# Performance work log

Measured on AMD Instinct MI355X. Metric: run time of the kernel, lower is better.

The kernel has to match this reference:

```python
import jax, jax.numpy as jnp
import numpy as np

EPS = 1e-5

def _conv1d(x, w, b):
    # x: [B, T, Cin]; w: [Cout, Cin, K] (torch layout); padding=1, stride=1
    y = jax.lax.conv_general_dilated(
        x, jnp.transpose(w, (2, 1, 0)), window_strides=(1,), padding=[(1, 1)],
        dimension_numbers=('NWC', 'WIO', 'NWC'))
    return y + b

def _layernorm(x, g, b):
    mu = jnp.mean(x, axis=-1, keepdims=True)
    var = jnp.mean(jnp.square(x - mu), axis=-1, keepdims=True)
    return (x - mu) * jax.lax.rsqrt(var + EPS) * g + b

def _predictor(x, conv1_w, conv1_b, ln1_g, ln1_b, conv2_w, conv2_b, ln2_g, ln2_b, lin_w, lin_b):
    h = _layernorm(jax.nn.relu(_conv1d(x, conv1_w, conv1_b)), ln1_g, ln1_b)
    h = _layernorm(jax.nn.relu(_conv1d(h, conv2_w, conv2_b)), ln2_g, ln2_b)
    # linear to 1 channel, relu, squeeze -> [B, T]
    return jax.nn.relu(jnp.einsum('btf,f->bt', h, lin_w[:, 0]) + lin_b[0])

def _length_regulate(x, durations, mel_max_length):
    # Equivalent to the one-hot alignment matmul: output frame p of batch b
    # copies token k where cumsum(dur)[k-1] <= p < cumsum(dur)[k]; zeros beyond total.
    B, T, D = x.shape
    cum = jnp.cumsum(durations, axis=-1)                       # [B, T]
    frames = jnp.arange(mel_max_length, dtype=cum.dtype)       # [M]
    idx = jax.vmap(lambda c: jnp.searchsorted(c, frames, side='right'))(cum)  # [B, M]
    idx = jnp.clip(idx, 0, T - 1)
    out = jnp.take_along_axis(x, idx[..., None], axis=1)       # [B, M, D]
    mask = (frames[None, :] < cum[:, -1:])                     # [B, M]
    return out * mask[..., None].astype(x.dtype)

def setup_inputs() -> dict:
    key = jax.random.key(0)
    ks = jax.random.split(key, 8)
    B, T, D, F = 32, 512, 256, 256
    M = 3584  # mel_max_length >= max possible sum of durations (7 * 512)
    x = jax.random.normal(ks[0], (B, T, D), dtype=jnp.float32)
    target = jax.random.randint(ks[1], (B, T), 0, 8, dtype=jnp.int32)
    s = 0.02
    return {
        'x': x,
        'conv1_w': jax.random.normal(ks[2], (F, D, 3), jnp.float32) * s,
        'conv1_b': jnp.zeros((F,), jnp.float32),
        'ln1_g': jnp.ones((F,), jnp.float32),
        'ln1_b': jnp.zeros((F,), jnp.float32),
        'conv2_w': jax.random.normal(ks[3], (F, F, 3), jnp.float32) * s,
        'conv2_b': jnp.zeros((F,), jnp.float32),
        'ln2_g': jnp.ones((F,), jnp.float32),
        'ln2_b': jnp.zeros((F,), jnp.float32),
        'lin_w': jax.random.normal(ks[4], (F, 1), jnp.float32) * s,
        'lin_b': jnp.zeros((1,), jnp.float32),
        'target': target,
        'mel_max_length': M,
    }

def reference(x, conv1_w, conv1_b, ln1_g, ln1_b, conv2_w, conv2_b, ln2_g, ln2_b, lin_w, lin_b, target, mel_max_length):
    dur_pred = _predictor(x, conv1_w, conv1_b, ln1_g, ln1_b, conv2_w, conv2_b, ln2_g, ln2_b, lin_w, lin_b)
    output = _length_regulate(x, target, mel_max_length)
    return output, dur_pred
```

## Files before the change

kernel.cpp:

```cpp
#include <hip/hip_runtime.h>
#include <hip/hip_bf16.h>

typedef float f32x4 __attribute__((ext_vector_type(4)));
typedef __bf16 bf16x8 __attribute__((ext_vector_type(8)));

static __device__ __forceinline__ unsigned short f2bf(float f) {
    unsigned int u = __float_as_uint(f);
    unsigned int r = (u + 0x7fffu + ((u >> 16) & 1u)) >> 16;
    return (unsigned short)r;
}

static __device__ __forceinline__ void gll16(const void* g, void* l) {
    __builtin_amdgcn_global_load_lds(
        (const __attribute__((address_space(1))) unsigned int*)g,
        (__attribute__((address_space(3))) unsigned int*)l, 16, 0, 0);
}

__global__ __launch_bounds__(512) void prep(
    const float* __restrict__ w1, const float* __restrict__ w2,
    unsigned short* __restrict__ w1p, unsigned short* __restrict__ w2p,
    const int* __restrict__ tgt, short* __restrict__ idxT, int M)
{
    int blk = blockIdx.x;
    if (blk < 768) {
        int gi = blk * 512 + threadIdx.x;
        const float* w = (gi < 196608) ? w1 : w2;
        unsigned short* wp = (gi < 196608) ? w1p : w2p;
        int j = (gi < 196608) ? gi : gi - 196608;
        int e = j & 7;
        int ch = j >> 3;
        int kt = ch >> 10;
        int rem = ch & 1023;
        int nb = rem >> 6, l = rem & 63;
        int n = nb * 16 + (l & 15);
        int cin = (kt & 7) * 32 + (l >> 4) * 8 + e;
        int kk = kt >> 3;
        wp[j] = f2bf(w[n * 768 + cin * 3 + kk]);
    } else {
        __shared__ int s[512];
        int b = blk - 768, tid = threadIdx.x;
        int d = tgt[b * 512 + tid];
        s[tid] = d;
        __syncthreads();
        for (int off = 1; off < 512; off <<= 1) {
            int v = (tid >= off) ? s[tid - off] : 0;
            __syncthreads();
            s[tid] += v;
            __syncthreads();
        }
        int myend = s[tid];
        int mystart = myend - d;
        short* row = idxT + (size_t)b * M;
        for (int p = mystart; p < myend; ++p) row[p] = (short)tid;
        __syncthreads();
        int total = s[511];
        for (int p = total + tid; p < M; p += 512) row[p] = (short)-1;
    }
}

static __device__ __forceinline__ void gather_part(
    int gblk, int phase, const float* __restrict__ x, const short* __restrict__ idxT,
    float* __restrict__ out, int M, int wv, int lane)
{
    int b = gblk / 56;
    int r0 = (gblk % 56) * 32 + phase;
    const short* row = idxT + (size_t)b * M;
    int id[4];
    #pragma unroll
    for (int i = 0; i < 4; ++i) id[i] = row[r0 + i * 8 + wv];
    #pragma unroll
    for (int i = 0; i < 4; ++i) {
        int m = r0 + i * 8 + wv;
        float4 v = make_float4(0.f, 0.f, 0.f, 0.f);
        if (id[i] >= 0)
            v = *reinterpret_cast<const float4*>(x + ((size_t)(b * 512 + id[i])) * 256 + lane * 4);
        *reinterpret_cast<float4*>(out + ((size_t)b * M + m) * 256 + lane * 4) = v;
    }
}

__global__ __launch_bounds__(512, 4) void conv1_hetero(
    const float* __restrict__ x, const unsigned short* __restrict__ Wp,
    const float* __restrict__ bias, const float* __restrict__ g,
    const float* __restrict__ be, unsigned short* __restrict__ h1b,
    const short* __restrict__ idxT, float* __restrict__ out, int M)
{
    __shared__ __align__(16) unsigned short As[66 * 256];
    __shared__ __align__(16) unsigned short Bsm[2][8192];
    __shared__ float lnS[4][64], lnQ[4][64];

    const int tid = threadIdx.x;
    const int lane = tid & 63;
    const int wv = tid >> 6;

    if (blockIdx.x >= 256) {
        gather_part(blockIdx.x - 256, 0, x, idxT, out, M, wv, lane);
        return;
    }

    const int wmi = wv >> 2, wni = wv & 3;
    const int grp = lane >> 4, lr = lane & 15;
    const int b = blockIdx.x >> 3;
    const int t_base = (blockIdx.x & 7) * 64;

    #pragma unroll
    for (int i = 0; i < 9; ++i) {
        int cc = i * 512 + tid;
        if (cc < 66 * 64) {
            int row = cc >> 6, q = cc & 63;
            int tt = t_base - 1 + row;
            ushort4 o = make_ushort4(0, 0, 0, 0);
            if ((unsigned)tt < 512u) {
                float4 v = *reinterpret_cast<const float4*>(x + ((size_t)(b * 512 + tt)) * 256 + q * 4);
                o.x = f2bf(v.x); o.y = f2bf(v.y); o.z = f2bf(v.z); o.w = f2bf(v.w);
            }
            *reinterpret_cast<ushort4*>(&As[row * 256 + ((q * 4) ^ ((row & 7) << 3))]) = o;
        }
    }

    const char* wpB = (const char*)Wp;
    char* bs0 = (char*)&Bsm[0][0];
    #define STAGE_B(kt, buf) do {                                              \
        const char* _s = wpB + (kt) * 16384 + wv * 2048 + lane * 16;           \
        char* _d = bs0 + (buf) * 16384 + wv * 2048;                            \
        gll16(_s, _d); gll16(_s + 1024, _d + 1024);                            \
    } while (0)

    STAGE_B(0, 0);
    __syncthreads();

    f32x4 acc[2][4] = {};
    int cur = 0;
    for (int kt = 0; kt < 24; ++kt) {
        if (kt < 23) STAGE_B(kt + 1, cur ^ 1);
        const int kk = kt >> 3, cin0 = (kt & 7) * 32;
        bf16x8 af[2], bfr[4];
        #pragma unroll
        for (int mi = 0; mi < 2; ++mi) {
            int tr = wmi * 32 + mi * 16 + lr + kk;
            af[mi] = *reinterpret_cast<const bf16x8*>(&As[tr * 256 + ((cin0 + grp * 8) ^ ((tr & 7) << 3))]);
        }
        #pragma unroll
        for (int ni = 0; ni < 4; ++ni)
            bfr[ni] = *reinterpret_cast<const bf16x8*>(&Bsm[cur][(wni * 4 + ni) * 512 + lane * 8]);
        __builtin_amdgcn_s_setprio(1);
        #pragma unroll
        for (int mi = 0; mi < 2; ++mi)
            #pragma unroll
            for (int ni = 0; ni < 4; ++ni)
                acc[mi][ni] = __builtin_amdgcn_mfma_f32_16x16x32_bf16(af[mi], bfr[ni], acc[mi][ni], 0, 0, 0);
        __builtin_amdgcn_s_setprio(0);
        __syncthreads();
        cur ^= 1;
    }

    float bcol[4], gcol[4], becol[4];
    #pragma unroll
    for (int ni = 0; ni < 4; ++ni) {
        int col = wni * 64 + ni * 16 + lr;
        bcol[ni] = bias[col]; gcol[ni] = g[col]; becol[ni] = be[col];
    }
    #pragma unroll
    for (int mi = 0; mi < 2; ++mi)
        #pragma unroll
        for (int ni = 0; ni < 4; ++ni)
            #pragma unroll
            for (int r = 0; r < 4; ++r)
                acc[mi][ni][r] = fmaxf(acc[mi][ni][r] + bcol[ni], 0.f);

    #pragma unroll
    for (int mi = 0; mi < 2; ++mi)
        #pragma unroll
        for (int r = 0; r < 4; ++r) {
            float s = acc[mi][0][r] + acc[mi][1][r] + acc[mi][2][r] + acc[mi][3][r];
            float q = acc[mi][0][r] * acc[mi][0][r] + acc[mi][1][r] * acc[mi][1][r]
                    + acc[mi][2][r] * acc[mi][2][r] + acc[mi][3][r] * acc[mi][3][r];
            #pragma unroll
            for (int off = 1; off < 16; off <<= 1) {
                s += __shfl_xor(s, off);
                q += __shfl_xor(q, off);
            }
            if (lr == 0) {
                int R = wmi * 32 + mi * 16 + grp * 4 + r;
                lnS[wni][R] = s; lnQ[wni][R] = q;
            }
        }
    __syncthreads();

    unsigned short* Hs = &Bsm[0][0];
    #pragma unroll
    for (int mi = 0; mi < 2; ++mi)
        #pragma unroll
        for (int r = 0; r < 4; ++r) {
            int R = wmi * 32 + mi * 16 + grp * 4 + r;
            float mu = (lnS[0][R] + lnS[1][R] + lnS[2][R] + lnS[3][R]) * (1.f / 256.f);
            float var = (lnQ[0][R] + lnQ[1][R] + lnQ[2][R] + lnQ[3][R]) * (1.f / 256.f) - mu * mu;
            float rs = rsqrtf(var + 1e-5f);
            #pragma unroll
            for (int ni = 0; ni < 4; ++ni) {
                int col = wni * 64 + ni * 16 + lr;
                float h = (acc[mi][ni][r] - mu) * rs * gcol[ni] + becol[ni];
                Hs[R * 256 + (col ^ ((R & 7) << 3))] = f2bf(h);
            }
        }
    __syncthreads();
    #pragma unroll
    for (int i = 0; i < 4; ++i) {
        int c = i * 512 + tid;
        int row = c >> 5, seg = c & 31;
        uint4 v = *reinterpret_cast<const uint4*>(&Hs[row * 256 + seg * 8]);
        *reinterpret_cast<uint4*>(h1b + ((size_t)(b * 512 + t_base + row)) * 256 + seg * 8) = v;
    }
    #undef STAGE_B
}

__global__ __launch_bounds__(512, 4) void conv2_hetero(
    const unsigned short* __restrict__ h1b, const unsigned short* __restrict__ Wp,
    const float* __restrict__ bias, const float* __restrict__ g,
    const float* __restrict__ be, const float* __restrict__ lw,
    const float* __restrict__ lb, float* __restrict__ dur,
    const short* __restrict__ idxT, const float* __restrict__ x,
    float* __restrict__ out, int M)
{
    __shared__ __align__(16) unsigned short As[66 * 256];
    __shared__ __align__(16) unsigned short Bsm[2][8192];
    __shared__ float lnS[4][64], lnQ[4][64], lnD[4][64];

    const int tid = threadIdx.x;
    const int lane = tid & 63;
    const int wv = tid >> 6;

    if (blockIdx.x >= 256) {
        gather_part(blockIdx.x - 256, 1792, x, idxT, out, M, wv, lane);
        return;
    }

    const int wmi = wv >> 2, wni = wv & 3;
    const int grp = lane >> 4, lr = lane & 15;
    const int b = blockIdx.x >> 3;
    const int t_base = (blockIdx.x & 7) * 64;

    {
        const char* src = (const char*)h1b + ((size_t)(b * 512 + t_base)) * 512 + wv * 4096 + lane * 16;
        char* dst = (char*)&As[256] + wv * 4096;
        #pragma unroll
        for (int i = 0; i < 4; ++i) gll16(src + i * 1024, dst + i * 1024);
    }
    if (tid < 32) {
        int tt = t_base - 1;
        uint4 v = make_uint4(0u, 0u, 0u, 0u);
        if (tt >= 0)
            v = *reinterpret_cast<const uint4*>((const char*)h1b + ((size_t)(b * 512 + tt)) * 512 + tid * 16);
        *reinterpret_cast<uint4*>((char*)As + tid * 16) = v;
    } else if (tid < 64) {
        int t2 = tid - 32, tt = t_base + 64;
        uint4 v = make_uint4(0u, 0u, 0u, 0u);
        if (tt < 512)
            v = *reinterpret_cast<const uint4*>((const char*)h1b + ((size_t)(b * 512 + tt)) * 512 + t2 * 16);
        *reinterpret_cast<uint4*>((char*)&As[65 * 256] + t2 * 16) = v;
    }

    const char* wpB = (const char*)Wp;
    char* bs0 = (char*)&Bsm[0][0];
    #define STAGE_B(kt, buf) do {                                              \
        const char* _s = wpB + (kt) * 16384 + wv * 2048 + lane * 16;           \
        char* _d = bs0 + (buf) * 16384 + wv * 2048;                            \
        gll16(_s, _d); gll16(_s + 1024, _d + 1024);                            \
    } while (0)

    STAGE_B(0, 0);
    __syncthreads();

    f32x4 acc[2][4] = {};
    int cur = 0;
    for (int kt = 0; kt < 24; ++kt) {
        if (kt < 23) STAGE_B(kt + 1, cur ^ 1);
        const int kk = kt >> 3, cin0 = (kt & 7) * 32;
        bf16x8 af[2], bfr[4];
        #pragma unroll
        for (int mi = 0; mi < 2; ++mi) {
            int tr = wmi * 32 + mi * 16 + lr + kk;
            af[mi] = *reinterpret_cast<const bf16x8*>(&As[tr * 256 + ((cin0 + grp * 8) ^ (((tr + 7) & 7) << 3))]);
        }
        #pragma unroll
        for (int ni = 0; ni < 4; ++ni)
            bfr[ni] = *reinterpret_cast<const bf16x8*>(&Bsm[cur][(wni * 4 + ni) * 512 + lane * 8]);
        __builtin_amdgcn_s_setprio(1);
        #pragma unroll
        for (int mi = 0; mi < 2; ++mi)
            #pragma unroll
            for (int ni = 0; ni < 4; ++ni)
                acc[mi][ni] = __builtin_amdgcn_mfma_f32_16x16x32_bf16(af[mi], bfr[ni], acc[mi][ni], 0, 0, 0);
        __builtin_amdgcn_s_setprio(0);
        __syncthreads();
        cur ^= 1;
    }

    float bcol[4], gcol[4], becol[4], wcol[4];
    #pragma unroll
    for (int ni = 0; ni < 4; ++ni) {
        int col = wni * 64 + ni * 16 + lr;
        bcol[ni] = bias[col]; gcol[ni] = g[col]; becol[ni] = be[col]; wcol[ni] = lw[col];
    }
    #pragma unroll
    for (int mi = 0; mi < 2; ++mi)
        #pragma unroll
        for (int ni = 0; ni < 4; ++ni)
            #pragma unroll
            for (int r = 0; r < 4; ++r)
                acc[mi][ni][r] = fmaxf(acc[mi][ni][r] + bcol[ni], 0.f);

    #pragma unroll
    for (int mi = 0; mi < 2; ++mi)
        #pragma unroll
        for (int r = 0; r < 4; ++r) {
            float s = acc[mi][0][r] + acc[mi][1][r] + acc[mi][2][r] + acc[mi][3][r];
            float q = acc[mi][0][r] * acc[mi][0][r] + acc[mi][1][r] * acc[mi][1][r]
                    + acc[mi][2][r] * acc[mi][2][r] + acc[mi][3][r] * acc[mi][3][r];
            #pragma unroll
            for (int off = 1; off < 16; off <<= 1) {
                s += __shfl_xor(s, off);
                q += __shfl_xor(q, off);
            }
            if (lr == 0) {
                int R = wmi * 32 + mi * 16 + grp * 4 + r;
                lnS[wni][R] = s; lnQ[wni][R] = q;
            }
        }
    __syncthreads();
    #pragma unroll
    for (int mi = 0; mi < 2; ++mi)
        #pragma unroll
        for (int r = 0; r < 4; ++r) {
            int R = wmi * 32 + mi * 16 + grp * 4 + r;
            float mu = (lnS[0][R] + lnS[1][R] + lnS[2][R] + lnS[3][R]) * (1.f / 256.f);
            float var = (lnQ[0][R] + lnQ[1][R] + lnQ[2][R] + lnQ[3][R]) * (1.f / 256.f) - mu * mu;
            float rs = rsqrtf(var + 1e-5f);
            float d = ((acc[mi][0][r] - mu) * rs * gcol[0] + becol[0]) * wcol[0]
                    + ((acc[mi][1][r] - mu) * rs * gcol[1] + becol[1]) * wcol[1]
                    + ((acc[mi][2][r] - mu) * rs * gcol[2] + becol[2]) * wcol[2]
                    + ((acc[mi][3][r] - mu) * rs * gcol[3] + becol[3]) * wcol[3];
            #pragma unroll
            for (int off = 1; off < 16; off <<= 1) d += __shfl_xor(d, off);
            if (lr == 0) lnD[wni][R] = d;
        }
    __syncthreads();
    if (tid < 64) {
        float dd = lnD[0][tid] + lnD[1][tid] + lnD[2][tid] + lnD[3][tid] + lb[0];
        dur[(size_t)b * 512 + t_base + tid] = fmaxf(dd, 0.f);
    }
    #undef STAGE_B
}

extern "C" void kernel_launch(void* const* d_in, const int* in_sizes, int n_in,
                              void* d_out, int out_size, void* d_ws, size_t ws_size,
                              hipStream_t stream) {
    const float* x   = (const float*)d_in[0];
    const float* w1  = (const float*)d_in[1];
    const float* b1  = (const float*)d_in[2];
    const float* g1  = (const float*)d_in[3];
    const float* be1 = (const float*)d_in[4];
    const float* w2  = (const float*)d_in[5];
    const float* b2  = (const float*)d_in[6];
    const float* g2  = (const float*)d_in[7];
    const float* be2 = (const float*)d_in[8];
    const float* lw  = (const float*)d_in[9];
    const float* lb  = (const float*)d_in[10];
    const int* tgt   = (const int*)d_in[11];
    float* out = (float*)d_out;

    const int B = 32, T = 512, C = 256;
    const int rows = B * T;
    const int M = (out_size - rows) / (B * C);

    char* ws = (char*)d_ws;
    unsigned short* w1p = (unsigned short*)(ws);
    unsigned short* w2p = (unsigned short*)(ws + 393216);
    unsigned short* h1b = (unsigned short*)(ws + 786432);
    short* idxT         = (short*)(ws + 9175040);

    prep<<<800, 512, 0, stream>>>(w1, w2, w1p, w2p, tgt, idxT, M);
    conv1_hetero<<<2048, 512, 0, stream>>>(x, w1p, b1, g1, be1, h1b, idxT, out, M);
    conv2_hetero<<<2048, 512, 0, stream>>>(h1b, w2p, b2, g2, be2, lw, lb,
                                           out + (size_t)B * M * C, idxT, x, out, M);
}
```

Baseline: 58.49 us.

## Single-buffer weight tiles for higher occupancy, coalesce weight prep, nontemporal gather stores

```diff
diff --git a/kernel.cpp b/kernel.cpp
--- a/kernel.cpp
+++ b/kernel.cpp
@@ -22,23 +22,23 @@
     const int* __restrict__ tgt, short* __restrict__ idxT, int M)
 {
     int blk = blockIdx.x;
-    if (blk < 768) {
+    if (blk < 256) {
         int gi = blk * 512 + threadIdx.x;
-        const float* w = (gi < 196608) ? w1 : w2;
-        unsigned short* wp = (gi < 196608) ? w1p : w2p;
-        int j = (gi < 196608) ? gi : gi - 196608;
-        int e = j & 7;
-        int ch = j >> 3;
-        int kt = ch >> 10;
-        int rem = ch & 1023;
-        int nb = rem >> 6, l = rem & 63;
-        int n = nb * 16 + (l & 15);
-        int cin = (kt & 7) * 32 + (l >> 4) * 8 + e;
-        int kk = kt >> 3;
-        wp[j] = f2bf(w[n * 768 + cin * 3 + kk]);
+        const float* w = (gi < 65536) ? w1 : w2;
+        unsigned short* wp = (gi < 65536) ? w1p : w2p;
+        int p = gi & 65535;
+        int n = p >> 8, cin = p & 255;
+        const float* src = w + (size_t)p * 3;
+        float a[3] = {src[0], src[1], src[2]};
+        int nb = n >> 4, nl = n & 15;
+        int e = cin & 7, lhi = (cin >> 3) & 3, chi = cin >> 5;
+        int base = nb * 512 + (lhi * 16 + nl) * 8 + e;
+        #pragma unroll
+        for (int kk = 0; kk < 3; ++kk)
+            wp[(kk * 8 + chi) * 8192 + base] = f2bf(a[kk]);
     } else {
         __shared__ int s[512];
-        int b = blk - 768, tid = threadIdx.x;
+        int b = blk - 256, tid = threadIdx.x;
         int d = tgt[b * 512 + tid];
         s[tid] = d;
         __syncthreads();
@@ -71,21 +71,22 @@
     #pragma unroll
     for (int i = 0; i < 4; ++i) {
         int m = r0 + i * 8 + wv;
-        float4 v = make_float4(0.f, 0.f, 0.f, 0.f);
+        f32x4 v = {0.f, 0.f, 0.f, 0.f};
         if (id[i] >= 0)
-            v = *reinterpret_cast<const float4*>(x + ((size_t)(b * 512 + id[i])) * 256 + lane * 4);
-        *reinterpret_cast<float4*>(out + ((size_t)b * M + m) * 256 + lane * 4) = v;
-    }
-}
-
-__global__ __launch_bounds__(512, 4) void conv1_hetero(
+            v = *reinterpret_cast<const f32x4*>(x + ((size_t)(b * 512 + id[i])) * 256 + lane * 4);
+        __builtin_nontemporal_store(
+            v, reinterpret_cast<f32x4*>(out + ((size_t)b * M + m) * 256 + lane * 4));
+    }
+}
+
+__global__ __launch_bounds__(512, 6) void conv1_hetero(
     const float* __restrict__ x, const unsigned short* __restrict__ Wp,
     const float* __restrict__ bias, const float* __restrict__ g,
     const float* __restrict__ be, unsigned short* __restrict__ h1b,
     const short* __restrict__ idxT, float* __restrict__ out, int M)
 {
     __shared__ __align__(16) unsigned short As[66 * 256];
-    __shared__ __align__(16) unsigned short Bsm[2][8192];
+    __shared__ __align__(16) unsigned short Bs[8192];
     __shared__ float lnS[4][64], lnQ[4][64];
 
     const int tid = threadIdx.x;
@@ -118,20 +119,17 @@
     }
 
     const char* wpB = (const char*)Wp;
-    char* bs0 = (char*)&Bsm[0][0];
-    #define STAGE_B(kt, buf) do {                                              \
+    #define STAGE_B(kt) do {                                                   \
         const char* _s = wpB + (kt) * 16384 + wv * 2048 + lane * 16;           \
-        char* _d = bs0 + (buf) * 16384 + wv * 2048;                            \
+        char* _d = (char*)Bs + wv * 2048;                                      \
         gll16(_s, _d); gll16(_s + 1024, _d + 1024);                            \
     } while (0)
 
-    STAGE_B(0, 0);
-    __syncthreads();
-
     f32x4 acc[2][4] = {};
-    int cur = 0;
     for (int kt = 0; kt < 24; ++kt) {
-        if (kt < 23) STAGE_B(kt + 1, cur ^ 1);
+        __syncthreads();
+        STAGE_B(kt);
+        __syncthreads();
         const int kk = kt >> 3, cin0 = (kt & 7) * 32;
         bf16x8 af[2], bfr[4];
         #pragma unroll
@@ -141,7 +139,7 @@
         }
         #pragma unroll
         for (int ni = 0; ni < 4; ++ni)
-            bfr[ni] = *reinterpret_cast<const bf16x8*>(&Bsm[cur][(wni * 4 + ni) * 512 + lane * 8]);
+            bfr[ni] = *reinterpret_cast<const bf16x8*>(&Bs[(wni * 4 + ni) * 512 + lane * 8]);
         __builtin_amdgcn_s_setprio(1);
         #pragma unroll
         for (int mi = 0; mi < 2; ++mi)
@@ -149,8 +147,6 @@
             for (int ni = 0; ni < 4; ++ni)
                 acc[mi][ni] = __builtin_amdgcn_mfma_f32_16x16x32_bf16(af[mi], bfr[ni], acc[mi][ni], 0, 0, 0);
         __builtin_amdgcn_s_setprio(0);
-        __syncthreads();
-        cur ^= 1;
     }
 
     float bcol[4], gcol[4], becol[4];
@@ -186,7 +182,7 @@
         }
     __syncthreads();
 
-    unsigned short* Hs = &Bsm[0][0];
+    unsigned short* Hs = As;
     #pragma unroll
     for (int mi = 0; mi < 2; ++mi)
         #pragma unroll
@@ -213,7 +209,7 @@
     #undef STAGE_B
 }
 
-__global__ __launch_bounds__(512, 4) void conv2_hetero(
+__global__ __launch_bounds__(512, 6) void conv2_hetero(
     const unsigned short* __restrict__ h1b, const unsigned short* __restrict__ Wp,
     const float* __restrict__ bias, const float* __restrict__ g,
     const float* __restrict__ be, const float* __restrict__ lw,
@@ -222,7 +218,7 @@
     float* __restrict__ out, int M)
 {
     __shared__ __align__(16) unsigned short As[66 * 256];
-    __shared__ __align__(16) unsigned short Bsm[2][8192];
+    __shared__ __align__(16) unsigned short Bs[8192];
     __shared__ float lnS[4][64], lnQ[4][64], lnD[4][64];
 
     const int tid = threadIdx.x;
@@ -260,20 +256,17 @@
     }
 
     const char* wpB = (const char*)Wp;
-    char* bs0 = (char*)&Bsm[0][0];
-    #define STAGE_B(kt, buf) do {                                              \
+    #define STAGE_B(kt) do {                                                   \
         const char* _s = wpB + (kt) * 16384 + wv * 2048 + lane * 16;           \
-        char* _d = bs0 + (buf) * 16384 + wv * 2048;                            \
+        char* _d = (char*)Bs + wv * 2048;                                      \
         gll16(_s, _d); gll16(_s + 1024, _d + 1024);                            \
     } while (0)
 
-    STAGE_B(0, 0);
-    __syncthreads();
-
     f32x4 acc[2][4] = {};
-    int cur = 0;
     for (int kt = 0; kt < 24; ++kt) {
-        if (kt < 23) STAGE_B(kt + 1, cur ^ 1);
+        __syncthreads();
+        STAGE_B(kt);
+        __syncthreads();
         const int kk = kt >> 3, cin0 = (kt & 7) * 32;
         bf16x8 af[2], bfr[4];
         #pragma unroll
@@ -283,7 +276,7 @@
         }
         #pragma unroll
         for (int ni = 0; ni < 4; ++ni)
-            bfr[ni] = *reinterpret_cast<const bf16x8*>(&Bsm[cur][(wni * 4 + ni) * 512 + lane * 8]);
+            bfr[ni] = *reinterpret_cast<const bf16x8*>(&Bs[(wni * 4 + ni) * 512 + lane * 8]);
         __builtin_amdgcn_s_setprio(1);
         #pragma unroll
         for (int mi = 0; mi < 2; ++mi)
@@ -291,8 +284,6 @@
             for (int ni = 0; ni < 4; ++ni)
                 acc[mi][ni] = __builtin_amdgcn_mfma_f32_16x16x32_bf16(af[mi], bfr[ni], acc[mi][ni], 0, 0, 0);
         __builtin_amdgcn_s_setprio(0);
-        __syncthreads();
-        cur ^= 1;
     }
 
     float bcol[4], gcol[4], becol[4], wcol[4];
@@ -378,7 +369,7 @@
     unsigned short* h1b = (unsigned short*)(ws + 786432);
     short* idxT         = (short*)(ws + 9175040);
 
-    prep<<<800, 512, 0, stream>>>(w1, w2, w1p, w2p, tgt, idxT, M);
+    prep<<<288, 512, 0, stream>>>(w1, w2, w1p, w2p, tgt, idxT, M);
     conv1_hetero<<<2048, 512, 0, stream>>>(x, w1p, b1, g1, be1, h1b, idxT, out, M);
     conv2_hetero<<<2048, 512, 0, stream>>>(h1b, w2p, b2, g2, be2, lw, lb,
                                            out + (size_t)B * M * C, idxT, x, out, M);
```

After: 63.09 us. 1.08x slower.
